# Optimization experiments

Hardware: AMD Instinct MI355X
Metric: run time of the kernel (lower is better)

Reference implementation:

```python
import jax, jax.numpy as jnp
import numpy as np

N = 100000   # nodes
E = 1000000  # edges
F_IN = 64    # in_ch
HID = 64     # hid_ch
CLS = 32     # num_classes


def _linear_params(key, out_dim, in_dim):
    kw, kb = jax.random.split(key)
    w = jax.random.normal(kw, (out_dim, in_dim), dtype=jnp.float32) * 0.05
    b = jax.random.normal(kb, (out_dim,), dtype=jnp.float32) * 0.05
    return w, b


def setup_inputs() -> dict:
    key = jax.random.key(0)
    ks = jax.random.split(key, 9)
    x = jax.random.normal(ks[0], (N, F_IN), dtype=jnp.float32)
    edge_index = jax.random.randint(ks[1], (2, E), 0, N, dtype=jnp.int64)
    # conv1: pre Linear(2F->F), post Linear(4F->HID), lin Linear(HID->HID)
    W1_pre, b1_pre = _linear_params(ks[2], F_IN, 2 * F_IN)
    W1_post, b1_post = _linear_params(ks[3], HID, 4 * F_IN)
    W1_lin, b1_lin = _linear_params(ks[4], HID, HID)
    # conv2: pre Linear(2H->H), post Linear(4H->HID), lin Linear(HID->HID)
    W2_pre, b2_pre = _linear_params(ks[5], HID, 2 * HID)
    W2_post, b2_post = _linear_params(ks[6], HID, 4 * HID)
    W2_lin, b2_lin = _linear_params(ks[7], HID, HID)
    # final classifier Linear(HID->CLS)
    Wf, bf = _linear_params(ks[8], CLS, HID)
    return {
        "x": x, "edge_index": edge_index,
        "W1_pre": W1_pre, "b1_pre": b1_pre, "W1_post": W1_post, "b1_post": b1_post,
        "W1_lin": W1_lin, "b1_lin": b1_lin,
        "W2_pre": W2_pre, "b2_pre": b2_pre, "W2_post": W2_post, "b2_post": b2_post,
        "W2_lin": W2_lin, "b2_lin": b2_lin,
        "Wf": Wf, "bf": bf,
    }


def _pna_conv(x, src, dst, Wpre, bpre, Wpost, bpost, Wlin, blin):
    """PyG PNAConv (towers=1, pre/post_layers=1, scalers=['identity'])."""
    n = x.shape[0]
    # message: pre_nn(cat([x_i, x_j]))  (i = target = dst, j = source = src)
    h = jnp.concatenate([x[dst], x[src]], axis=-1)  # [E, 2F]
    m = h @ Wpre.T + bpre                            # [E, F]
    # multi-aggregation at target nodes: mean, max, sum
    s = jax.ops.segment_sum(m, dst, num_segments=n)                    # [N, F]
    cnt = jax.ops.segment_sum(jnp.ones((m.shape[0],), m.dtype), dst,
                              num_segments=n)                          # [N]
    mean = s / jnp.maximum(cnt, 1.0)[:, None]
    mx = jax.ops.segment_max(m, dst, num_segments=n)
    mx = jnp.where(jnp.isfinite(mx), mx, jnp.zeros_like(mx))  # empty -> 0 (PyG)
    agg = jnp.concatenate([mean, mx, s], axis=-1)              # [N, 3F]
    out = jnp.concatenate([x, agg], axis=-1) @ Wpost.T + bpost # [N, HID]
    return out @ Wlin.T + blin


def reference(x, edge_index, W1_pre, b1_pre, W1_post, b1_post, W1_lin, b1_lin,
              W2_pre, b2_pre, W2_post, b2_post, W2_lin, b2_lin, Wf, bf):
    src = edge_index[0]
    dst = edge_index[1]
    h = jax.nn.relu(_pna_conv(x, src, dst, W1_pre, b1_pre, W1_post, b1_post,
                              W1_lin, b1_lin))
    h = jax.nn.relu(_pna_conv(h, src, dst, W2_pre, b2_pre, W2_post, b2_post,
                              W2_lin, b2_lin))
    return h @ Wf.T + bf  # [N, CLS]
```

## Files before the change

### kernel.cpp

```cpp
#include <hip/hip_runtime.h>

#define NN 100000
#define NE 1000000
#define NCLS 32
#define NB 391
#define GN 32
#define NGROUPS (NN/GN)
#define UVG ((NN+63)/64)

typedef __bf16 bf16x8 __attribute__((ext_vector_type(8)));
typedef float f32x16 __attribute__((ext_vector_type(16)));

__device__ __forceinline__ unsigned pk_hi(unsigned u1, unsigned u0){
  return __builtin_amdgcn_perm(u1, u0, 0x07060302u);
}
__device__ __forceinline__ unsigned pk_lo(float f0, float f1, unsigned u0, unsigned u1){
  float r0 = f0 - __uint_as_float(u0 & 0xFFFF0000u);
  float r1 = f1 - __uint_as_float(u1 & 0xFFFF0000u);
  return pk_hi(__float_as_uint(r1), __float_as_uint(r0));
}
__device__ __forceinline__ f32x16 mfma_b(uint4 a, uint4 b, f32x16 c){
  bf16x8 av, bv;
  __builtin_memcpy(&av, &a, 16);
  __builtin_memcpy(&bv, &b, 16);
  return __builtin_amdgcn_mfma_f32_32x32x16_bf16(av, bv, c, 0, 0, 0);
}
__device__ __forceinline__ int crow(int r, int half){ return (r&3) + 8*(r>>2) + 4*half; }

__global__ void k_setup(const float* __restrict__ W1_lin, const float* __restrict__ b1_lin,
                        const float* __restrict__ W1_post, const float* __restrict__ b1_post,
                        const float* __restrict__ W2_lin, const float* __restrict__ b2_lin,
                        const float* __restrict__ W2_post, const float* __restrict__ b2_post,
                        const float* __restrict__ W1_pre, const float* __restrict__ W2_pre,
                        const float* __restrict__ Wf,
                        uint4* __restrict__ Wcf, uint4* __restrict__ Wpf,
                        uint4* __restrict__ Wff, float* __restrict__ bc,
                        int* __restrict__ deg){
  const int blk = blockIdx.x, tid = threadIdx.x;
  if (blk < 16){
    int i = blk*256 + tid;
    int layer = i >> 11;
    int t = (i >> 10) & 1, step = (i >> 6) & 15, lane = i & 63;
    const float* Wlin  = layer ? W2_lin  : W1_lin;
    const float* Wpost = layer ? W2_post : W1_post;
    int col = t*32 + (lane & 31);
    int k0 = step*16 + ((lane >> 5) << 3);
    unsigned hi[4], lo[4];
    for (int p = 0; p < 4; p++){
      float f0 = 0.f, f1 = 0.f;
      for (int j = 0; j < 64; j++){
        float wl = Wlin[col*64 + j];
        f0 += wl * Wpost[j*256 + k0 + 2*p];
        f1 += wl * Wpost[j*256 + k0 + 2*p + 1];
      }
      unsigned u0 = __float_as_uint(f0), u1 = __float_as_uint(f1);
      hi[p] = pk_hi(u1, u0);
      lo[p] = pk_lo(f0, f1, u0, u1);
    }
    uint4* base = Wcf + layer*4096;
    base[t*1024     + step*64 + lane] = make_uint4(hi[0],hi[1],hi[2],hi[3]);
    base[(2+t)*1024 + step*64 + lane] = make_uint4(lo[0],lo[1],lo[2],lo[3]);
  } else if (blk < 24){
    int i = (blk-16)*256 + tid;
    int layer = i >> 10;
    int t = (i >> 8) & 3, st = (i >> 6) & 3, lane = i & 63;
    const float* Wpre = layer ? W2_pre : W1_pre;
    int col = t*32 + (lane & 31);
    int o = col & 63, koff = (col >> 6) * 64;
    int k0 = st*16 + ((lane >> 5) << 3);
    unsigned hi[4], lo[4];
    for (int p = 0; p < 4; p++){
      float f0 = Wpre[o*128 + koff + k0 + 2*p];
      float f1 = Wpre[o*128 + koff + k0 + 2*p + 1];
      unsigned u0 = __float_as_uint(f0), u1 = __float_as_uint(f1);
      hi[p] = pk_hi(u1, u0);
      lo[p] = pk_lo(f0, f1, u0, u1);
    }
    uint4* base = Wpf + layer*2048 + t*512;
    base[st*64 + lane]       = make_uint4(hi[0],hi[1],hi[2],hi[3]);
    base[256 + st*64 + lane] = make_uint4(lo[0],lo[1],lo[2],lo[3]);
  } else if (blk == 24){
    int st = tid >> 6, lane = tid & 63;
    int cls = lane & 31;
    int k0 = st*16 + ((lane >> 5) << 3);
    unsigned hi[4], lo[4];
    for (int p = 0; p < 4; p++){
      float f0 = Wf[cls*64 + k0 + 2*p];
      float f1 = Wf[cls*64 + k0 + 2*p + 1];
      unsigned u0 = __float_as_uint(f0), u1 = __float_as_uint(f1);
      hi[p] = pk_hi(u1, u0);
      lo[p] = pk_lo(f0, f1, u0, u1);
    }
    Wff[st*64 + lane]       = make_uint4(hi[0],hi[1],hi[2],hi[3]);
    Wff[256 + st*64 + lane] = make_uint4(lo[0],lo[1],lo[2],lo[3]);
  } else if (blk == 25){
    if (tid < 128){
      int layer = tid >> 6, o = tid & 63;
      const float* Wlin  = layer ? W2_lin  : W1_lin;
      const float* blin  = layer ? b2_lin  : b1_lin;
      const float* bpost = layer ? b2_post : b1_post;
      float s = blin[o];
      for (int j = 0; j < 64; j++) s += Wlin[o*64+j] * bpost[j];
      bc[tid] = s;
    }
  } else {
    int i = (blk-26)*256 + tid;
    if (i < NN) deg[i] = 0;
  }
}

__global__ void k_deg(const int* __restrict__ dst, int* __restrict__ deg){
  int e = blockIdx.x*256 + threadIdx.x;
  if (e < NE) atomicAdd(&deg[dst[e]], 1);
}

__global__ void k_scan1(const int* __restrict__ deg, int* __restrict__ inc,
                        int* __restrict__ part){
  __shared__ int s[256];
  int tid = threadIdx.x;
  int i = blockIdx.x*256 + tid;
  s[tid] = (i < NN) ? deg[i] : 0;
  __syncthreads();
  for (int off = 1; off < 256; off <<= 1){
    int t = (tid >= off) ? s[tid-off] : 0;
    __syncthreads();
    s[tid] += t;
    __syncthreads();
  }
  inc[i] = s[tid];
  if (tid == 255) part[blockIdx.x] = s[255];
}

__global__ void k_scan23(const int* __restrict__ inc, const int* __restrict__ part,
                         const int* __restrict__ deg,
                         int* __restrict__ rowptr, int* __restrict__ cursor){
  __shared__ int s[512];
  int tid = threadIdx.x;
  s[tid] = (tid < NB) ? part[tid] : 0;
  __syncthreads();
  for (int off = 1; off < 512; off <<= 1){
    int t = (tid >= off) ? s[tid-off] : 0;
    __syncthreads();
    s[tid] += t;
    __syncthreads();
  }
  int b = blockIdx.x;
  int base = b ? s[b-1] : 0;
  if (tid < 256){
    int i = b*256 + tid;
    if (i < NN){
      int inclusive = inc[i] + base;
      rowptr[i+1] = inclusive;
      cursor[i] = inclusive - deg[i];
    }
  }
  if (b == 0 && tid == 0) rowptr[0] = 0;
}

__global__ void k_scatter(const int* __restrict__ src, const int* __restrict__ dst,
                          int* __restrict__ cursor, int* __restrict__ srcs){
  int e = blockIdx.x*256 + threadIdx.x;
  if (e < NE){
    int d = dst[e];
    int p = atomicAdd(&cursor[d], 1);
    srcs[p] = src[e];
  }
}

__global__ __launch_bounds__(512, 4) void k_uv(
    const float* __restrict__ xin, const uint4* __restrict__ Wpf,
    const float* __restrict__ bpre, float* __restrict__ u, unsigned* __restrict__ vq){
  __shared__ __align__(16) unsigned XH[64*36];
  __shared__ __align__(16) unsigned XL[64*36];
  const int tid = threadIdx.x;
  const int lane = tid & 63;
  const int w = tid >> 6;
  const int t = w >> 1, rg = w & 1;
  const int cc = lane & 31, half = lane >> 5;
  const int col = t*32 + cc;
  uint4 wfr[2][4];
  {
    const uint4* p = Wpf + t*512;
    #pragma unroll
    for (int s = 0; s < 2; s++)
      #pragma unroll
      for (int st = 0; st < 4; st++) wfr[s][st] = p[s*256 + st*64 + lane];
  }
  const float bias = (t < 2) ? bpre[col] : 0.f;
  const int dcol = col & 63;
  const int srow = tid >> 3, sq = tid & 7;

  for (int g = blockIdx.x; g < UVG; g += gridDim.x){
    const int n0 = g*64;
    __syncthreads();
    {
      const int node = n0 + srow;
      float4 a = {0,0,0,0}, b = {0,0,0,0};
      if (node < NN){
        a = *(const float4*)&xin[(size_t)node*64 + sq*8];
        b = *(const float4*)&xin[(size_t)node*64 + sq*8 + 4];
      }
      unsigned ax = __float_as_uint(a.x), ay = __float_as_uint(a.y);
      unsigned az = __float_as_uint(a.z), aw = __float_as_uint(a.w);
      unsigned bx = __float_as_uint(b.x), by = __float_as_uint(b.y);
      unsigned bz = __float_as_uint(b.z), bw = __float_as_uint(b.w);
      uint4 hi, lo;
      hi.x = pk_hi(ay, ax); lo.x = pk_lo(a.x, a.y, ax, ay);
      hi.y = pk_hi(aw, az); lo.y = pk_lo(a.z, a.w, az, aw);
      hi.z = pk_hi(by, bx); lo.z = pk_lo(b.x, b.y, bx, by);
      hi.w = pk_hi(bw, bz); lo.w = pk_lo(b.z, b.w, bz, bw);
      *(uint4*)&XH[srow*36 + sq*4] = hi;
      *(uint4*)&XL[srow*36 + sq*4] = lo;
    }
    __syncthreads();
    f32x16 acc = {};
    const int arow = (rg*32 + cc)*36 + half*4;
    #pragma unroll
    for (int st = 0; st < 4; st++){
      uint4 ah = *(const uint4*)&XH[arow + st*8];
      uint4 al = *(const uint4*)&XL[arow + st*8];
      acc = mfma_b(ah, wfr[0][st], acc);
      acc = mfma_b(al, wfr[0][st], acc);
      acc = mfma_b(ah, wfr[1][st], acc);
    }
    if (t < 2){
      #pragma unroll
      for (int r = 0; r < 16; r++){
        int row = n0 + rg*32 + crow(r, half);
        if (row < NN) u[(size_t)row*64 + dcol] = acc[r] + bias;
      }
    } else {
      #pragma unroll
      for (int r = 0; r < 16; r++){
        float val = acc[r];
        float pv = __shfl_xor(val, 1, 64);
        if ((cc & 1) == 0){
          unsigned pk;
          asm("v_cvt_pk_bf16_f32 %0, %1, %2" : "=v"(pk) : "v"(val), "v"(pv));
          int row = n0 + rg*32 + crow(r, half);
          if (row < NN) vq[(size_t)row*32 + (dcol >> 1)] = pk;
        }
      }
    }
  }
}

template<int EPI>
__global__ __launch_bounds__(512, 8) void k_agg(
    const float* __restrict__ xin, const float* __restrict__ u,
    const unsigned* __restrict__ vq,
    const int* __restrict__ rowptr, const int* __restrict__ srcs,
    const uint4* __restrict__ Wcf, const float* __restrict__ bcv,
    const uint4* __restrict__ Wff, const float* __restrict__ bfv,
    float* __restrict__ hout, float* __restrict__ outp){
  __shared__ __align__(16) unsigned Zh[GN*132];
  __shared__ __align__(16) unsigned Zl[GN*132];
  const int tid = threadIdx.x;
  const int lane = tid & 63;
  const int w = tid >> 6;
  const int c = lane & 31;
  const int h = lane >> 5;
  const float bias = (w < 2) ? bcv[w*32 + c] : 0.f;
  const uint4* WH = Wcf + w*1024;
  const uint4* WL = Wcf + (2+w)*1024;

  for (int g = blockIdx.x; g < NGROUPS; g += gridDim.x){
    const int n0 = g*GN;
    __syncthreads();
    #pragma unroll
    for (int pr = 0; pr < 2; pr++){
      const int nA = n0 + w*4 + pr*2;
      const int r0A = rowptr[nA],   r1A = rowptr[nA+1];
      const int r0B = rowptr[nA+1], r1B = rowptr[nA+2];
      int jA = r0A + h, jB = r0B + h;
      int a0=0,a1=0,a2=0,a3=0, b0=0,b1=0,b2=0,b3=0;
      bool hA = (jA + 6 < r1A), hB = (jB + 6 < r1B);
      if (hA){ a0=srcs[jA]; a1=srcs[jA+2]; a2=srcs[jA+4]; a3=srcs[jA+6]; }
      if (hB){ b0=srcs[jB]; b1=srcs[jB+2]; b2=srcs[jB+4]; b3=srcs[jB+6]; }
      #pragma unroll
      for (int sub = 0; sub < 2; sub++){
        const int node = nA + sub;
        const int r1 = sub ? r1B : r1A;
        int jj = sub ? jB : jA;
        int e0 = sub?b0:a0, e1 = sub?b1:a1, e2 = sub?b2:a2, e3 = sub?b3:a3;
        bool have = sub ? hB : hA;
        float Sx = 0.f, Sy = 0.f;
        float Mx = -3.402823466e+38f, My = Mx;
        while (have){
          int njj = jj + 8;
          bool more = (njj + 6 < r1);
          int f0=0,f1=0,f2=0,f3=0;
          if (more){ f0=srcs[njj]; f1=srcs[njj+2]; f2=srcs[njj+4]; f3=srcs[njj+6]; }
          unsigned p0 = vq[(size_t)e0*32 + c];
          unsigned p1 = vq[(size_t)e1*32 + c];
          unsigned p2 = vq[(size_t)e2*32 + c];
          unsigned p3 = vq[(size_t)e3*32 + c];
          float x0 = __uint_as_float(p0 << 16), y0 = __uint_as_float(p0 & 0xFFFF0000u);
          float x1 = __uint_as_float(p1 << 16), y1 = __uint_as_float(p1 & 0xFFFF0000u);
          float x2 = __uint_as_float(p2 << 16), y2 = __uint_as_float(p2 & 0xFFFF0000u);
          float x3 = __uint_as_float(p3 << 16), y3 = __uint_as_float(p3 & 0xFFFF0000u);
          Sx += (x0 + x1) + (x2 + x3);
          Sy += (y0 + y1) + (y2 + y3);
          Mx = fmaxf(Mx, fmaxf(fmaxf(x0, x1), fmaxf(x2, x3)));
          My = fmaxf(My, fmaxf(fmaxf(y0, y1), fmaxf(y2, y3)));
          jj = njj; e0=f0; e1=f1; e2=f2; e3=f3; have = more;
        }
        for (; jj < r1; jj += 2){
          unsigned p = vq[(size_t)srcs[jj]*32 + c];
          float x0 = __uint_as_float(p << 16), y0 = __uint_as_float(p & 0xFFFF0000u);
          Sx += x0; Sy += y0;
          Mx = fmaxf(Mx, x0); My = fmaxf(My, y0);
        }
        Sx += __shfl_xor(Sx, 32, 64);
        Sy += __shfl_xor(Sy, 32, 64);
        Mx = fmaxf(Mx, __shfl_xor(Mx, 32, 64));
        My = fmaxf(My, __shfl_xor(My, 32, 64));

        const float2 up = *(const float2*)&u[(size_t)node*64 + 2*c];
        const float2 xv = *(const float2*)&xin[(size_t)node*64 + 2*c];
        const int d = r1 - (sub ? r0B : r0A);
        float2 z1, z2, z3;
        if (d > 0){
          float fd = (float)d;
          z1.x = up.x + Sx/fd;  z1.y = up.y + Sy/fd;
          z2.x = up.x + Mx;     z2.y = up.y + My;
          z3.x = fmaf(fd, up.x, Sx); z3.y = fmaf(fd, up.y, Sy);
        } else {
          z1.x=z1.y=z2.x=z2.y=z3.x=z3.y=0.f;
        }
        const int row = w*4 + pr*2 + sub;
        float2 q[4] = {xv, z1, z2, z3};
        #pragma unroll
        for (int qq = 0; qq < 4; qq++){
          unsigned u0 = __float_as_uint(q[qq].x), u1 = __float_as_uint(q[qq].y);
          if (h == 0) Zh[row*132 + qq*32 + c] = pk_hi(u1, u0);
          else        Zl[row*132 + qq*32 + c] = pk_lo(q[qq].x, q[qq].y, u0, u1);
        }
      }
    }
    __syncthreads();
    f32x16 acc = {};
    if (w < 2){
      const int arow = c*132 + h*4;
      #pragma unroll 4
      for (int s = 0; s < 16; s++){
        uint4 ah = *(const uint4*)&Zh[arow + s*8];
        uint4 al = *(const uint4*)&Zl[arow + s*8];
        uint4 bh = WH[s*64 + lane];
        uint4 bl = WL[s*64 + lane];
        acc = mfma_b(ah, bh, acc);
        acc = mfma_b(al, bh, acc);
        acc = mfma_b(ah, bl, acc);
      }
      if (EPI == 0){
        #pragma unroll
        for (int r = 0; r < 16; r++){
          float val = fmaxf(acc[r] + bias, 0.f);
          hout[(size_t)(n0 + crow(r,h))*64 + w*32 + c] = val;
        }
      }
    }
    if (EPI == 1){
      __syncthreads();
      if (w < 2){
        float* HF = (float*)Zh;
        #pragma unroll
        for (int r = 0; r < 16; r++){
          float val = fmaxf(acc[r] + bias, 0.f);
          HF[crow(r,h)*64 + w*32 + c] = val;
        }
      }
      __syncthreads();
      {
        const float* HF = (const float*)Zh;
        unsigned* HH = Zl;
        unsigned* HL = Zl + 1152;
        const int row = tid >> 4, p4 = tid & 15;
        float4 f = *(const float4*)&HF[row*64 + p4*4];
        unsigned f0 = __float_as_uint(f.x), f1 = __float_as_uint(f.y);
        unsigned f2 = __float_as_uint(f.z), f3 = __float_as_uint(f.w);
        HH[row*36 + p4*2]   = pk_hi(f1, f0);
        HH[row*36 + p4*2+1] = pk_hi(f3, f2);
        HL[row*36 + p4*2]   = pk_lo(f.x, f.y, f0, f1);
        HL[row*36 + p4*2+1] = pk_lo(f.z, f.w, f2, f3);
      }
      __syncthreads();
      if (w == 0){
        f32x16 ac2 = {};
        const unsigned* HH = Zl;
        const unsigned* HL = Zl + 1152;
        const int arow = c*36 + h*4;
        #pragma unroll
        for (int st = 0; st < 4; st++){
          uint4 ah = *(const uint4*)&HH[arow + st*8];
          uint4 al = *(const uint4*)&HL[arow + st*8];
          uint4 bh = Wff[st*64 + lane];
          uint4 bl = Wff[256 + st*64 + lane];
          ac2 = mfma_b(ah, bh, ac2);
          ac2 = mfma_b(al, bh, ac2);
          ac2 = mfma_b(ah, bl, ac2);
        }
        const float bcls = bfv[c];
        #pragma unroll
        for (int r = 0; r < 16; r++)
          outp[(size_t)(n0 + crow(r,h))*NCLS + c] = ac2[r] + bcls;
      }
    }
  }
}

extern "C" void kernel_launch(void* const* d_in, const int* in_sizes, int n_in,
                              void* d_out, int out_size, void* d_ws, size_t ws_size,
                              hipStream_t stream){
  const float* x      = (const float*)d_in[0];
  const int*   ei     = (const int*)  d_in[1];
  const int*   src    = ei;
  const int*   dst    = ei + NE;
  const float* W1_pre = (const float*)d_in[2];
  const float* b1_pre = (const float*)d_in[3];
  const float* W1_post= (const float*)d_in[4];
  const float* b1_post= (const float*)d_in[5];
  const float* W1_lin = (const float*)d_in[6];
  const float* b1_lin = (const float*)d_in[7];
  const float* W2_pre = (const float*)d_in[8];
  const float* b2_pre = (const float*)d_in[9];
  const float* W2_post= (const float*)d_in[10];
  const float* b2_post= (const float*)d_in[11];
  const float* W2_lin = (const float*)d_in[12];
  const float* b2_lin = (const float*)d_in[13];
  const float* Wf     = (const float*)d_in[14];
  const float* bf     = (const float*)d_in[15];
  float* out = (float*)d_out;

  size_t off = 0;
  char* ws = (char*)d_ws;
  auto alloc = [&](size_t bytes){ void* p = ws + off; off += (bytes + 255) & ~(size_t)255; return p; };
  int*      deg    = (int*)     alloc(NN*4);
  int*      rowptr = (int*)     alloc((NN+1)*4);
  int*      cursor = (int*)     alloc(NN*4);
  int*      inc    = (int*)     alloc(NB*256*4);
  int*      part   = (int*)     alloc(512*4);
  int*      srcs   = (int*)     alloc((size_t)NE*4);
  float*    u      = (float*)   alloc((size_t)NN*64*4);
  unsigned* vq     = (unsigned*)alloc((size_t)NN*32*4);
  float*    h1     = (float*)   alloc((size_t)NN*64*4);
  uint4*    Wcf    = (uint4*)   alloc(2*4096*16);
  uint4*    Wpf    = (uint4*)   alloc(4096*16);
  uint4*    Wff    = (uint4*)   alloc(512*16);
  float*    bc     = (float*)   alloc(128*4);

  k_setup<<<417, 256, 0, stream>>>(W1_lin, b1_lin, W1_post, b1_post,
                                   W2_lin, b2_lin, W2_post, b2_post,
                                   W1_pre, W2_pre, Wf, Wcf, Wpf, Wff, bc, deg);
  k_deg    <<<(NE+255)/256, 256, 0, stream>>>(dst, deg);
  k_scan1  <<<NB, 256, 0, stream>>>(deg, inc, part);
  k_scan23 <<<NB, 512, 0, stream>>>(inc, part, deg, rowptr, cursor);
  k_scatter<<<(NE+255)/256, 256, 0, stream>>>(src, dst, cursor, srcs);

  k_uv    <<<1024, 512, 0, stream>>>(x, Wpf, b1_pre, u, vq);
  k_agg<0><<<2048, 512, 0, stream>>>(x, u, vq, rowptr, srcs, Wcf, bc,
                                     nullptr, nullptr, h1, nullptr);

  k_uv    <<<1024, 512, 0, stream>>>(h1, Wpf + 2048, b2_pre, u, vq);
  k_agg<1><<<2048, 512, 0, stream>>>(h1, u, vq, rowptr, srcs, Wcf + 4096, bc + 64,
                                     Wff, bf, nullptr, out);
}
```

Measured before the change: 310.0 us.

## Interleave two nodes' neighbor gathers with clamped indices, launch one block per group

The per-wave aggregation now processes the two nodes' edge lists in one interleaved loop. It clamps indices to the last edge and masks the sums, so every batch issues four gathers with no scalar remainder loop, which raises memory-level parallelism and removes divergent tail handling. Max needs no mask because the clamped duplicates are real neighbors. Launch grids change from fixed counts to one block per node group or per 64 nodes. The cost is redundant loads on partial batches and more registers held live.

```diff
diff --git a/kernel.cpp b/kernel.cpp
--- a/kernel.cpp
+++ b/kernel.cpp
@@ -10,6 +10,8 @@
 
 typedef __bf16 bf16x8 __attribute__((ext_vector_type(8)));
 typedef float f32x16 __attribute__((ext_vector_type(16)));
+
+__device__ __forceinline__ int imin(int a, int b){ return a < b ? a : b; }
 
 __device__ __forceinline__ unsigned pk_hi(unsigned u1, unsigned u0){
   return __builtin_amdgcn_perm(u1, u0, 0x07060302u);
@@ -263,6 +265,7 @@
   const float bias = (w < 2) ? bcv[w*32 + c] : 0.f;
   const uint4* WH = Wcf + w*1024;
   const uint4* WL = Wcf + (2+w)*1024;
+  const float NINF = -3.402823466e+38f;
 
   for (int g = blockIdx.x; g < NGROUPS; g += gridDim.x){
     const int n0 = g*GN;
@@ -272,53 +275,82 @@
       const int nA = n0 + w*4 + pr*2;
       const int r0A = rowptr[nA],   r1A = rowptr[nA+1];
       const int r0B = rowptr[nA+1], r1B = rowptr[nA+2];
-      int jA = r0A + h, jB = r0B + h;
-      int a0=0,a1=0,a2=0,a3=0, b0=0,b1=0,b2=0,b3=0;
-      bool hA = (jA + 6 < r1A), hB = (jB + 6 < r1B);
-      if (hA){ a0=srcs[jA]; a1=srcs[jA+2]; a2=srcs[jA+4]; a3=srcs[jA+6]; }
-      if (hB){ b0=srcs[jB]; b1=srcs[jB+2]; b2=srcs[jB+4]; b3=srcs[jB+6]; }
-      #pragma unroll
-      for (int sub = 0; sub < 2; sub++){
-        const int node = nA + sub;
-        const int r1 = sub ? r1B : r1A;
-        int jj = sub ? jB : jA;
-        int e0 = sub?b0:a0, e1 = sub?b1:a1, e2 = sub?b2:a2, e3 = sub?b3:a3;
-        bool have = sub ? hB : hA;
-        float Sx = 0.f, Sy = 0.f;
-        float Mx = -3.402823466e+38f, My = Mx;
-        while (have){
-          int njj = jj + 8;
-          bool more = (njj + 6 < r1);
-          int f0=0,f1=0,f2=0,f3=0;
-          if (more){ f0=srcs[njj]; f1=srcs[njj+2]; f2=srcs[njj+4]; f3=srcs[njj+6]; }
-          unsigned p0 = vq[(size_t)e0*32 + c];
-          unsigned p1 = vq[(size_t)e1*32 + c];
-          unsigned p2 = vq[(size_t)e2*32 + c];
-          unsigned p3 = vq[(size_t)e3*32 + c];
+      const int dA = r1A - r0A, dB = r1B - r0B;
+      const int nbA = (((dA + 1) >> 1) + 3) >> 2;
+      const int nbB = (((dB + 1) >> 1) + 3) >> 2;
+      const int nb  = nbA > nbB ? nbA : nbB;
+      const int jA0 = r0A + h, jB0 = r0B + h;
+      int iA0=0,iA1=0,iA2=0,iA3=0, iB0=0,iB1=0,iB2=0,iB3=0;
+      if (nbA){
+        int e1 = r1A - 1;
+        iA0 = srcs[imin(jA0,   e1)]; iA1 = srcs[imin(jA0+2, e1)];
+        iA2 = srcs[imin(jA0+4, e1)]; iA3 = srcs[imin(jA0+6, e1)];
+      }
+      if (nbB){
+        int e1 = r1B - 1;
+        iB0 = srcs[imin(jB0,   e1)]; iB1 = srcs[imin(jB0+2, e1)];
+        iB2 = srcs[imin(jB0+4, e1)]; iB3 = srcs[imin(jB0+6, e1)];
+      }
+      float SxA=0.f, SyA=0.f, MxA=NINF, MyA=NINF;
+      float SxB=0.f, SyB=0.f, MxB=NINF, MyB=NINF;
+      for (int t = 0; t < nb; t++){
+        if (t < nbA){
+          unsigned p0 = vq[(size_t)iA0*32 + c];
+          unsigned p1 = vq[(size_t)iA1*32 + c];
+          unsigned p2 = vq[(size_t)iA2*32 + c];
+          unsigned p3 = vq[(size_t)iA3*32 + c];
+          if (t+1 < nbA){
+            int jn = jA0 + 8*(t+1), e1 = r1A - 1;
+            iA0 = srcs[imin(jn,   e1)]; iA1 = srcs[imin(jn+2, e1)];
+            iA2 = srcs[imin(jn+4, e1)]; iA3 = srcs[imin(jn+6, e1)];
+          }
+          const int j = jA0 + 8*t;
           float x0 = __uint_as_float(p0 << 16), y0 = __uint_as_float(p0 & 0xFFFF0000u);
           float x1 = __uint_as_float(p1 << 16), y1 = __uint_as_float(p1 & 0xFFFF0000u);
           float x2 = __uint_as_float(p2 << 16), y2 = __uint_as_float(p2 & 0xFFFF0000u);
           float x3 = __uint_as_float(p3 << 16), y3 = __uint_as_float(p3 & 0xFFFF0000u);
-          Sx += (x0 + x1) + (x2 + x3);
-          Sy += (y0 + y1) + (y2 + y3);
-          Mx = fmaxf(Mx, fmaxf(fmaxf(x0, x1), fmaxf(x2, x3)));
-          My = fmaxf(My, fmaxf(fmaxf(y0, y1), fmaxf(y2, y3)));
-          jj = njj; e0=f0; e1=f1; e2=f2; e3=f3; have = more;
-        }
-        for (; jj < r1; jj += 2){
-          unsigned p = vq[(size_t)srcs[jj]*32 + c];
-          float x0 = __uint_as_float(p << 16), y0 = __uint_as_float(p & 0xFFFF0000u);
-          Sx += x0; Sy += y0;
-          Mx = fmaxf(Mx, x0); My = fmaxf(My, y0);
-        }
+          MxA = fmaxf(MxA, fmaxf(fmaxf(x0, x1), fmaxf(x2, x3)));
+          MyA = fmaxf(MyA, fmaxf(fmaxf(y0, y1), fmaxf(y2, y3)));
+          SxA += ((j   < r1A) ? x0 : 0.f) + ((j+2 < r1A) ? x1 : 0.f)
+               + ((j+4 < r1A) ? x2 : 0.f) + ((j+6 < r1A) ? x3 : 0.f);
+          SyA += ((j   < r1A) ? y0 : 0.f) + ((j+2 < r1A) ? y1 : 0.f)
+               + ((j+4 < r1A) ? y2 : 0.f) + ((j+6 < r1A) ? y3 : 0.f);
+        }
+        if (t < nbB){
+          unsigned p0 = vq[(size_t)iB0*32 + c];
+          unsigned p1 = vq[(size_t)iB1*32 + c];
+          unsigned p2 = vq[(size_t)iB2*32 + c];
+          unsigned p3 = vq[(size_t)iB3*32 + c];
+          if (t+1 < nbB){
+            int jn = jB0 + 8*(t+1), e1 = r1B - 1;
+            iB0 = srcs[imin(jn,   e1)]; iB1 = srcs[imin(jn+2, e1)];
+            iB2 = srcs[imin(jn+4, e1)]; iB3 = srcs[imin(jn+6, e1)];
+          }
+          const int j = jB0 + 8*t;
+          float x0 = __uint_as_float(p0 << 16), y0 = __uint_as_float(p0 & 0xFFFF0000u);
+          float x1 = __uint_as_float(p1 << 16), y1 = __uint_as_float(p1 & 0xFFFF0000u);
+          float x2 = __uint_as_float(p2 << 16), y2 = __uint_as_float(p2 & 0xFFFF0000u);
+          float x3 = __uint_as_float(p3 << 16), y3 = __uint_as_float(p3 & 0xFFFF0000u);
+          MxB = fmaxf(MxB, fmaxf(fmaxf(x0, x1), fmaxf(x2, x3)));
+          MyB = fmaxf(MyB, fmaxf(fmaxf(y0, y1), fmaxf(y2, y3)));
+          SxB += ((j   < r1B) ? x0 : 0.f) + ((j+2 < r1B) ? x1 : 0.f)
+               + ((j+4 < r1B) ? x2 : 0.f) + ((j+6 < r1B) ? x3 : 0.f);
+          SyB += ((j   < r1B) ? y0 : 0.f) + ((j+2 < r1B) ? y1 : 0.f)
+               + ((j+4 < r1B) ? y2 : 0.f) + ((j+6 < r1B) ? y3 : 0.f);
+        }
+      }
+      #pragma unroll
+      for (int sub = 0; sub < 2; sub++){
+        const int node = nA + sub;
+        const int d = sub ? dB : dA;
+        float Sx = sub ? SxB : SxA, Sy = sub ? SyB : SyA;
+        float Mx = sub ? MxB : MxA, My = sub ? MyB : MyA;
         Sx += __shfl_xor(Sx, 32, 64);
         Sy += __shfl_xor(Sy, 32, 64);
         Mx = fmaxf(Mx, __shfl_xor(Mx, 32, 64));
         My = fmaxf(My, __shfl_xor(My, 32, 64));
-
         const float2 up = *(const float2*)&u[(size_t)node*64 + 2*c];
         const float2 xv = *(const float2*)&xin[(size_t)node*64 + 2*c];
-        const int d = r1 - (sub ? r0B : r0A);
         float2 z1, z2, z3;
         if (d > 0){
           float fd = (float)d;
@@ -457,11 +489,11 @@
   k_scan23 <<<NB, 512, 0, stream>>>(inc, part, deg, rowptr, cursor);
   k_scatter<<<(NE+255)/256, 256, 0, stream>>>(src, dst, cursor, srcs);
 
-  k_uv    <<<1024, 512, 0, stream>>>(x, Wpf, b1_pre, u, vq);
-  k_agg<0><<<2048, 512, 0, stream>>>(x, u, vq, rowptr, srcs, Wcf, bc,
-                                     nullptr, nullptr, h1, nullptr);
-
-  k_uv    <<<1024, 512, 0, stream>>>(h1, Wpf + 2048, b2_pre, u, vq);
-  k_agg<1><<<2048, 512, 0, stream>>>(h1, u, vq, rowptr, srcs, Wcf + 4096, bc + 64,
-                                     Wff, bf, nullptr, out);
-}
+  k_uv    <<<UVG, 512, 0, stream>>>(x, Wpf, b1_pre, u, vq);
+  k_agg<0><<<NGROUPS, 512, 0, stream>>>(x, u, vq, rowptr, srcs, Wcf, bc,
+                                        nullptr, nullptr, h1, nullptr);
+
+  k_uv    <<<UVG, 512, 0, stream>>>(h1, Wpf + 2048, b2_pre, u, vq);
+  k_agg<1><<<NGROUPS, 512, 0, stream>>>(h1, u, vq, rowptr, srcs, Wcf + 4096, bc + 64,
+                                        Wff, bf, nullptr, out);
+}
```

Measured after the change: 298.4 us. 3.8% less time.

## Interleave neighbor gathers across four nodes per wave with clamped batched loads

Applied to the files above, without the earlier changes.

The aggregation loop now processes all four nodes assigned to a wave together in a single loop over batches. Each batch issues 16 independent gathers, with clamped duplicate indices standing in for a scalar tail loop, and masks the sum for padded slots. The goal is more memory-level parallelism and fewer divergent tail iterations, at the cost of higher register pressure and a few redundant loads. Grid sizes also change so that one block or group is launched per tile instead of using grid-stride loops.

```diff
diff --git a/kernel.cpp b/kernel.cpp
--- a/kernel.cpp
+++ b/kernel.cpp
@@ -10,6 +10,8 @@
 
 typedef __bf16 bf16x8 __attribute__((ext_vector_type(8)));
 typedef float f32x16 __attribute__((ext_vector_type(16)));
+
+__device__ __forceinline__ int imin(int a, int b){ return a < b ? a : b; }
 
 __device__ __forceinline__ unsigned pk_hi(unsigned u1, unsigned u0){
   return __builtin_amdgcn_perm(u1, u0, 0x07060302u);
@@ -263,72 +265,95 @@
   const float bias = (w < 2) ? bcv[w*32 + c] : 0.f;
   const uint4* WH = Wcf + w*1024;
   const uint4* WL = Wcf + (2+w)*1024;
+  const float NINF = -3.402823466e+38f;
 
   for (int g = blockIdx.x; g < NGROUPS; g += gridDim.x){
     const int n0 = g*GN;
     __syncthreads();
-    #pragma unroll
-    for (int pr = 0; pr < 2; pr++){
-      const int nA = n0 + w*4 + pr*2;
-      const int r0A = rowptr[nA],   r1A = rowptr[nA+1];
-      const int r0B = rowptr[nA+1], r1B = rowptr[nA+2];
-      int jA = r0A + h, jB = r0B + h;
-      int a0=0,a1=0,a2=0,a3=0, b0=0,b1=0,b2=0,b3=0;
-      bool hA = (jA + 6 < r1A), hB = (jB + 6 < r1B);
-      if (hA){ a0=srcs[jA]; a1=srcs[jA+2]; a2=srcs[jA+4]; a3=srcs[jA+6]; }
-      if (hB){ b0=srcs[jB]; b1=srcs[jB+2]; b2=srcs[jB+4]; b3=srcs[jB+6]; }
-      #pragma unroll
-      for (int sub = 0; sub < 2; sub++){
-        const int node = nA + sub;
-        const int r1 = sub ? r1B : r1A;
-        int jj = sub ? jB : jA;
-        int e0 = sub?b0:a0, e1 = sub?b1:a1, e2 = sub?b2:a2, e3 = sub?b3:a3;
-        bool have = sub ? hB : hA;
-        float Sx = 0.f, Sy = 0.f;
-        float Mx = -3.402823466e+38f, My = Mx;
-        while (have){
-          int njj = jj + 8;
-          bool more = (njj + 6 < r1);
-          int f0=0,f1=0,f2=0,f3=0;
-          if (more){ f0=srcs[njj]; f1=srcs[njj+2]; f2=srcs[njj+4]; f3=srcs[njj+6]; }
-          unsigned p0 = vq[(size_t)e0*32 + c];
-          unsigned p1 = vq[(size_t)e1*32 + c];
-          unsigned p2 = vq[(size_t)e2*32 + c];
-          unsigned p3 = vq[(size_t)e3*32 + c];
-          float x0 = __uint_as_float(p0 << 16), y0 = __uint_as_float(p0 & 0xFFFF0000u);
-          float x1 = __uint_as_float(p1 << 16), y1 = __uint_as_float(p1 & 0xFFFF0000u);
-          float x2 = __uint_as_float(p2 << 16), y2 = __uint_as_float(p2 & 0xFFFF0000u);
-          float x3 = __uint_as_float(p3 << 16), y3 = __uint_as_float(p3 & 0xFFFF0000u);
-          Sx += (x0 + x1) + (x2 + x3);
-          Sy += (y0 + y1) + (y2 + y3);
-          Mx = fmaxf(Mx, fmaxf(fmaxf(x0, x1), fmaxf(x2, x3)));
-          My = fmaxf(My, fmaxf(fmaxf(y0, y1), fmaxf(y2, y3)));
-          jj = njj; e0=f0; e1=f1; e2=f2; e3=f3; have = more;
-        }
-        for (; jj < r1; jj += 2){
-          unsigned p = vq[(size_t)srcs[jj]*32 + c];
-          float x0 = __uint_as_float(p << 16), y0 = __uint_as_float(p & 0xFFFF0000u);
-          Sx += x0; Sy += y0;
-          Mx = fmaxf(Mx, x0); My = fmaxf(My, y0);
-        }
-        Sx += __shfl_xor(Sx, 32, 64);
-        Sy += __shfl_xor(Sy, 32, 64);
-        Mx = fmaxf(Mx, __shfl_xor(Mx, 32, 64));
-        My = fmaxf(My, __shfl_xor(My, 32, 64));
-
+    {
+      const int nbase = n0 + w*4;
+      int r1a[4], ja[4], e1a[4], nb[4], da[4];
+      #pragma unroll
+      for (int n = 0; n < 4; n++){
+        int rr0 = rowptr[nbase + n], rr1 = rowptr[nbase + n + 1];
+        da[n] = rr1 - rr0;
+        r1a[n] = rr1;
+        e1a[n] = rr1 - 1;
+        ja[n] = rr0 + h;
+        nb[n] = (((da[n] + 1) >> 1) + 3) >> 2;
+      }
+      int idx[4][4];
+      #pragma unroll
+      for (int n = 0; n < 4; n++){
+        if (nb[n] > 0){
+          #pragma unroll
+          for (int s = 0; s < 4; s++)
+            idx[n][s] = srcs[imin(ja[n] + 2*s, e1a[n])];
+        }
+      }
+      float Sx[4], Sy[4], Mx[4], My[4];
+      #pragma unroll
+      for (int n = 0; n < 4; n++){ Sx[n]=0.f; Sy[n]=0.f; Mx[n]=NINF; My[n]=NINF; }
+      int nbmax = nb[0];
+      #pragma unroll
+      for (int n = 1; n < 4; n++) nbmax = nb[n] > nbmax ? nb[n] : nbmax;
+
+      for (int t = 0; t < nbmax; t++){
+        unsigned p[4][4];
+        #pragma unroll
+        for (int n = 0; n < 4; n++){
+          if (t < nb[n]){
+            #pragma unroll
+            for (int s = 0; s < 4; s++)
+              p[n][s] = vq[(size_t)idx[n][s]*32 + c];
+          }
+        }
+        #pragma unroll
+        for (int n = 0; n < 4; n++){
+          if (t + 1 < nb[n]){
+            int jn = ja[n] + 8*(t+1);
+            #pragma unroll
+            for (int s = 0; s < 4; s++)
+              idx[n][s] = srcs[imin(jn + 2*s, e1a[n])];
+          }
+        }
+        #pragma unroll
+        for (int n = 0; n < 4; n++){
+          if (t < nb[n]){
+            const int jb = ja[n] + 8*t;
+            float x0 = __uint_as_float(p[n][0] << 16), y0 = __uint_as_float(p[n][0] & 0xFFFF0000u);
+            float x1 = __uint_as_float(p[n][1] << 16), y1 = __uint_as_float(p[n][1] & 0xFFFF0000u);
+            float x2 = __uint_as_float(p[n][2] << 16), y2 = __uint_as_float(p[n][2] & 0xFFFF0000u);
+            float x3 = __uint_as_float(p[n][3] << 16), y3 = __uint_as_float(p[n][3] & 0xFFFF0000u);
+            Mx[n] = fmaxf(Mx[n], fmaxf(fmaxf(x0, x1), fmaxf(x2, x3)));
+            My[n] = fmaxf(My[n], fmaxf(fmaxf(y0, y1), fmaxf(y2, y3)));
+            Sx[n] += ((jb   < r1a[n]) ? x0 : 0.f) + ((jb+2 < r1a[n]) ? x1 : 0.f)
+                   + ((jb+4 < r1a[n]) ? x2 : 0.f) + ((jb+6 < r1a[n]) ? x3 : 0.f);
+            Sy[n] += ((jb   < r1a[n]) ? y0 : 0.f) + ((jb+2 < r1a[n]) ? y1 : 0.f)
+                   + ((jb+4 < r1a[n]) ? y2 : 0.f) + ((jb+6 < r1a[n]) ? y3 : 0.f);
+          }
+        }
+      }
+      #pragma unroll
+      for (int n = 0; n < 4; n++){
+        const int node = nbase + n;
+        float Sxv = Sx[n] + __shfl_xor(Sx[n], 32, 64);
+        float Syv = Sy[n] + __shfl_xor(Sy[n], 32, 64);
+        float Mxv = fmaxf(Mx[n], __shfl_xor(Mx[n], 32, 64));
+        float Myv = fmaxf(My[n], __shfl_xor(My[n], 32, 64));
         const float2 up = *(const float2*)&u[(size_t)node*64 + 2*c];
         const float2 xv = *(const float2*)&xin[(size_t)node*64 + 2*c];
-        const int d = r1 - (sub ? r0B : r0A);
+        const int d = da[n];
         float2 z1, z2, z3;
         if (d > 0){
           float fd = (float)d;
-          z1.x = up.x + Sx/fd;  z1.y = up.y + Sy/fd;
-          z2.x = up.x + Mx;     z2.y = up.y + My;
-          z3.x = fmaf(fd, up.x, Sx); z3.y = fmaf(fd, up.y, Sy);
+          z1.x = up.x + Sxv/fd;  z1.y = up.y + Syv/fd;
+          z2.x = up.x + Mxv;     z2.y = up.y + Myv;
+          z3.x = fmaf(fd, up.x, Sxv); z3.y = fmaf(fd, up.y, Syv);
         } else {
           z1.x=z1.y=z2.x=z2.y=z3.x=z3.y=0.f;
         }
-        const int row = w*4 + pr*2 + sub;
+        const int row = w*4 + n;
         float2 q[4] = {xv, z1, z2, z3};
         #pragma unroll
         for (int qq = 0; qq < 4; qq++){
@@ -457,11 +482,11 @@
   k_scan23 <<<NB, 512, 0, stream>>>(inc, part, deg, rowptr, cursor);
   k_scatter<<<(NE+255)/256, 256, 0, stream>>>(src, dst, cursor, srcs);
 
-  k_uv    <<<1024, 512, 0, stream>>>(x, Wpf, b1_pre, u, vq);
-  k_agg<0><<<2048, 512, 0, stream>>>(x, u, vq, rowptr, srcs, Wcf, bc,
-                                     nullptr, nullptr, h1, nullptr);
-
-  k_uv    <<<1024, 512, 0, stream>>>(h1, Wpf + 2048, b2_pre, u, vq);
-  k_agg<1><<<2048, 512, 0, stream>>>(h1, u, vq, rowptr, srcs, Wcf + 4096, bc + 64,
-                                     Wff, bf, nullptr, out);
-}
+  k_uv    <<<UVG, 512, 0, stream>>>(x, Wpf, b1_pre, u, vq);
+  k_agg<0><<<NGROUPS, 512, 0, stream>>>(x, u, vq, rowptr, srcs, Wcf, bc,
+                                        nullptr, nullptr, h1, nullptr);
+
+  k_uv    <<<UVG, 512, 0, stream>>>(h1, Wpf + 2048, b2_pre, u, vq);
+  k_agg<1><<<NGROUPS, 512, 0, stream>>>(h1, u, vq, rowptr, srcs, Wcf + 4096, bc + 64,
+                                        Wff, bf, nullptr, out);
+}
```

New measurement: 683.1 us. +120.4%, slower.

## Fuse layer-2 pre-projection into layer-1 aggregation epilogue

Applied to the files above, without the earlier changes.

Adds an EPI==2 variant of the aggregation kernel that, after computing layer-1 output h1 for a 32-node group, immediately applies the layer-2 pre-linear via MFMA and writes u2/vq2, removing the second k_uv launch and its re-read of h1. Double-buffered u/vq workspace is allocated when space permits, with a fallback to the old path. Grid sizes also change from fixed 1024/2048 to one block per group. Extra MFMA work and registers in the epilogue may reduce occupancy.

```diff
diff --git a/kernel.cpp b/kernel.cpp
--- a/kernel.cpp
+++ b/kernel.cpp
@@ -10,6 +10,8 @@
 
 typedef __bf16 bf16x8 __attribute__((ext_vector_type(8)));
 typedef float f32x16 __attribute__((ext_vector_type(16)));
+
+__device__ __forceinline__ int imin(int a, int b){ return a < b ? a : b; }
 
 __device__ __forceinline__ unsigned pk_hi(unsigned u1, unsigned u0){
   return __builtin_amdgcn_perm(u1, u0, 0x07060302u);
@@ -252,7 +254,9 @@
     const int* __restrict__ rowptr, const int* __restrict__ srcs,
     const uint4* __restrict__ Wcf, const float* __restrict__ bcv,
     const uint4* __restrict__ Wff, const float* __restrict__ bfv,
-    float* __restrict__ hout, float* __restrict__ outp){
+    const uint4* __restrict__ Wpf2, const float* __restrict__ bpre2,
+    float* __restrict__ hout, float* __restrict__ outp,
+    float* __restrict__ uout, unsigned* __restrict__ vqout){
   __shared__ __align__(16) unsigned Zh[GN*132];
   __shared__ __align__(16) unsigned Zl[GN*132];
   const int tid = threadIdx.x;
@@ -360,14 +364,16 @@
         }
       }
     }
-    if (EPI == 1){
+    if (EPI >= 1){
       __syncthreads();
       if (w < 2){
         float* HF = (float*)Zh;
         #pragma unroll
         for (int r = 0; r < 16; r++){
           float val = fmaxf(acc[r] + bias, 0.f);
-          HF[crow(r,h)*64 + w*32 + c] = val;
+          int rr = crow(r,h);
+          HF[rr*64 + w*32 + c] = val;
+          if (EPI == 2) hout[(size_t)(n0 + rr)*64 + w*32 + c] = val;
         }
       }
       __syncthreads();
@@ -385,25 +391,62 @@
         HL[row*36 + p4*2+1] = pk_lo(f.z, f.w, f2, f3);
       }
       __syncthreads();
-      if (w == 0){
-        f32x16 ac2 = {};
-        const unsigned* HH = Zl;
-        const unsigned* HL = Zl + 1152;
-        const int arow = c*36 + h*4;
-        #pragma unroll
-        for (int st = 0; st < 4; st++){
-          uint4 ah = *(const uint4*)&HH[arow + st*8];
-          uint4 al = *(const uint4*)&HL[arow + st*8];
-          uint4 bh = Wff[st*64 + lane];
-          uint4 bl = Wff[256 + st*64 + lane];
-          ac2 = mfma_b(ah, bh, ac2);
-          ac2 = mfma_b(al, bh, ac2);
-          ac2 = mfma_b(ah, bl, ac2);
-        }
-        const float bcls = bfv[c];
-        #pragma unroll
-        for (int r = 0; r < 16; r++)
-          outp[(size_t)(n0 + crow(r,h))*NCLS + c] = ac2[r] + bcls;
+      if (EPI == 1){
+        if (w == 0){
+          f32x16 ac2 = {};
+          const unsigned* HH = Zl;
+          const unsigned* HL = Zl + 1152;
+          const int arow = c*36 + h*4;
+          #pragma unroll
+          for (int st = 0; st < 4; st++){
+            uint4 ah = *(const uint4*)&HH[arow + st*8];
+            uint4 al = *(const uint4*)&HL[arow + st*8];
+            uint4 bh = Wff[st*64 + lane];
+            uint4 bl = Wff[256 + st*64 + lane];
+            ac2 = mfma_b(ah, bh, ac2);
+            ac2 = mfma_b(al, bh, ac2);
+            ac2 = mfma_b(ah, bl, ac2);
+          }
+          const float bcls = bfv[c];
+          #pragma unroll
+          for (int r = 0; r < 16; r++)
+            outp[(size_t)(n0 + crow(r,h))*NCLS + c] = ac2[r] + bcls;
+        }
+      } else if (EPI == 2){
+        if (w < 4){
+          f32x16 ac2 = {};
+          const unsigned* HH = Zl;
+          const unsigned* HL = Zl + 1152;
+          const int arow = c*36 + h*4;
+          const uint4* WB = Wpf2 + w*512;
+          #pragma unroll
+          for (int st = 0; st < 4; st++){
+            uint4 ah = *(const uint4*)&HH[arow + st*8];
+            uint4 al = *(const uint4*)&HL[arow + st*8];
+            uint4 bh = WB[st*64 + lane];
+            uint4 bl = WB[256 + st*64 + lane];
+            ac2 = mfma_b(ah, bh, ac2);
+            ac2 = mfma_b(al, bh, ac2);
+            ac2 = mfma_b(ah, bl, ac2);
+          }
+          if (w < 2){
+            const float b2 = bpre2[w*32 + c];
+            #pragma unroll
+            for (int r = 0; r < 16; r++)
+              uout[(size_t)(n0 + crow(r,h))*64 + w*32 + c] = ac2[r] + b2;
+          } else {
+            #pragma unroll
+            for (int r = 0; r < 16; r++){
+              float val = ac2[r];
+              float pv = __shfl_xor(val, 1, 64);
+              if ((c & 1) == 0){
+                unsigned pk;
+                asm("v_cvt_pk_bf16_f32 %0, %1, %2" : "=v"(pk) : "v"(val), "v"(pv));
+                vqout[(size_t)(n0 + crow(r,h))*32 + (w-2)*16 + (c >> 1)] = pk;
+              }
+            }
+          }
+        }
       }
     }
   }
@@ -448,6 +491,13 @@
   uint4*    Wpf    = (uint4*)   alloc(4096*16);
   uint4*    Wff    = (uint4*)   alloc(512*16);
   float*    bc     = (float*)   alloc(128*4);
+  bool fused = (off + (size_t)NN*64*4 + (size_t)NN*32*4 + 512 <= ws_size);
+  float*    u2  = u;
+  unsigned* vq2 = vq;
+  if (fused){
+    u2  = (float*)   alloc((size_t)NN*64*4);
+    vq2 = (unsigned*)alloc((size_t)NN*32*4);
+  }
 
   k_setup<<<417, 256, 0, stream>>>(W1_lin, b1_lin, W1_post, b1_post,
                                    W2_lin, b2_lin, W2_post, b2_post,
@@ -457,11 +507,19 @@
   k_scan23 <<<NB, 512, 0, stream>>>(inc, part, deg, rowptr, cursor);
   k_scatter<<<(NE+255)/256, 256, 0, stream>>>(src, dst, cursor, srcs);
 
-  k_uv    <<<1024, 512, 0, stream>>>(x, Wpf, b1_pre, u, vq);
-  k_agg<0><<<2048, 512, 0, stream>>>(x, u, vq, rowptr, srcs, Wcf, bc,
-                                     nullptr, nullptr, h1, nullptr);
-
-  k_uv    <<<1024, 512, 0, stream>>>(h1, Wpf + 2048, b2_pre, u, vq);
-  k_agg<1><<<2048, 512, 0, stream>>>(h1, u, vq, rowptr, srcs, Wcf + 4096, bc + 64,
-                                     Wff, bf, nullptr, out);
-}
+  k_uv<<<UVG, 512, 0, stream>>>(x, Wpf, b1_pre, u, vq);
+  if (fused){
+    k_agg<2><<<NGROUPS, 512, 0, stream>>>(x, u, vq, rowptr, srcs, Wcf, bc,
+                                          nullptr, nullptr, Wpf + 2048, b2_pre,
+                                          h1, nullptr, u2, vq2);
+  } else {
+    k_agg<0><<<NGROUPS, 512, 0, stream>>>(x, u, vq, rowptr, srcs, Wcf, bc,
+                                          nullptr, nullptr, nullptr, nullptr,
+                                          h1, nullptr, nullptr, nullptr);
+    k_uv<<<UVG, 512, 0, stream>>>(h1, Wpf + 2048, b2_pre, u2, vq2);
+  }
+
+  k_agg<1><<<NGROUPS, 512, 0, stream>>>(h1, u2, vq2, rowptr, srcs, Wcf + 4096, bc + 64,
+                                        Wff, bf, nullptr, nullptr,
+                                        nullptr, out, nullptr, nullptr);
+}
```

After: 368.8 us. 19.0% more time.
